# Kernel tuning notes

Hardware: AMD Instinct MI355X
Metric: run time of the kernel (lower is better)

The kernel has to match this reference:

```python
import jax, jax.numpy as jnp
import numpy as np

B, N, D, H = 4, 2048, 1024, 16
DH = D // H

def setup_inputs() -> dict:
    key = jax.random.key(0)
    kx, kqkv, ko = jax.random.split(key, 3)
    x = jax.random.normal(kx, (B, N, D), dtype=jnp.float32)
    # torch Linear weights: [out, in]; scale like default init
    W_qkv = jax.random.normal(kqkv, (3 * D, D), dtype=jnp.float32) * (1.0 / np.sqrt(D))
    W_out = jax.random.normal(ko, (D, D), dtype=jnp.float32) * (1.0 / np.sqrt(D))
    return {"x": x, "W_qkv": W_qkv, "W_out": W_out}

def reference(x, W_qkv, W_out):
    Bk, Nk, C = x.shape
    qkv = jnp.einsum('bnc,oc->bno', x, W_qkv)  # [B,N,3D]
    qkv = qkv.reshape(Bk, Nk, 3, H, DH).transpose(2, 0, 3, 1, 4)  # [3,B,H,N,DH]
    q, k, v = qkv[0], qkv[1], qkv[2]
    att = jnp.einsum('bhnd,bhmd->bhnm', q, k) * (1.0 / np.sqrt(DH))
    mask = jnp.triu(jnp.ones((Nk, Nk), dtype=bool), k=1)  # True above diagonal
    att = jnp.where(mask, -jnp.inf, att)
    att = jax.nn.softmax(att, axis=-1)
    y = jnp.einsum('bhnm,bhmd->bhnd', att, v)  # [B,H,N,DH]
    y = y.transpose(0, 2, 1, 3).reshape(Bk, Nk, C)
    return jnp.einsum('bnc,oc->bno', y, W_out)
```

## Files before the change

kernel.cpp:

```cpp
#include <hip/hip_runtime.h>
#include <hip/hip_bf16.h>
#include <stdint.h>

#define Bb 4
#define Nn 2048
#define Dd 1024
#define Hh 16
#define DHd 64
#define Mm (Bb*Nn)
#define D3 (3*Dd)

typedef unsigned short u16;
typedef unsigned int u32;
typedef __attribute__((ext_vector_type(8))) short bf16x8;
typedef __attribute__((ext_vector_type(4))) float f32x4;
typedef __attribute__((ext_vector_type(2))) unsigned int u32x2;
typedef __attribute__((ext_vector_type(4))) unsigned int u32x4;

__device__ __forceinline__ u16 f2bf(float f) {
    unsigned int u = __float_as_uint(f);
    u = (u + 0x7FFFu + ((u >> 16) & 1u)) >> 16;
    return (u16)u;
}

__device__ __forceinline__ u32 cvtpk_bf16(float lo, float hi) {
    u32 r;
    asm("v_cvt_pk_bf16_f32 %0, %1, %2" : "=v"(r) : "v"(lo), "v"(hi));
    return r;
}

__device__ __forceinline__ float fexp2(float x) {
    float r;
    asm("v_exp_f32 %0, %1" : "=v"(r) : "v"(x));
    return r;
}

#define GLOAD16(g, l)                                                          \
    __builtin_amdgcn_global_load_lds(                                          \
        (const __attribute__((address_space(1))) unsigned int*)(g),            \
        (__attribute__((address_space(3))) unsigned int*)(l), 16, 0, 0)

__global__ void cvt_all(const float* __restrict__ x, const float* __restrict__ wqkv,
                        const float* __restrict__ wout, u16* __restrict__ xb,
                        u16* __restrict__ wqkvb, u16* __restrict__ woutb, float s) {
    const int A4 = Mm * Dd / 4;
    const int B4 = D3 * Dd / 4;
    const int C4 = Dd * Dd / 4;
    const int QCUT = Dd * Dd / 4;
    const int total = A4 + B4 + C4;
    int i = blockIdx.x * blockDim.x + threadIdx.x;
    const int stride = gridDim.x * blockDim.x;
    for (; i < total; i += stride) {
        const float* src; u16* dst; int j; float sc = 1.f;
        if (i < A4) { src = x; dst = xb; j = i; }
        else if (i < A4 + B4) { j = i - A4; src = wqkv; dst = wqkvb; if (j < QCUT) sc = s; }
        else { j = i - A4 - B4; src = wout; dst = woutb; }
        float4 v = ((const float4*)src)[j];
        u16 o0 = f2bf(v.x * sc), o1 = f2bf(v.y * sc), o2 = f2bf(v.z * sc), o3 = f2bf(v.w * sc);
        ((uint2*)dst)[j] = make_uint2((u32)o0 | ((u32)o1 << 16), (u32)o2 | ((u32)o3 << 16));
    }
}

template<int OUT_F32>
__global__ __launch_bounds__(256) void gemm_bt(const u16* __restrict__ A,
                                               const u16* __restrict__ Bm,
                                               void* __restrict__ C,
                                               int M, int Nout, int K) {
    __shared__ u16 As[128 * 64];
    __shared__ u16 Bs[128 * 64];
    const int t = threadIdx.x;
    const int lane = t & 63;
    const int w = t >> 6;
    const int wr = w >> 1, wc = w & 1;
    const int l15 = lane & 15, l4 = lane >> 4;

    const int gx = gridDim.x;
    const int linear = blockIdx.y * gx + blockIdx.x;
    const int cpx = (gx * gridDim.y) >> 3;
    const int tile = (linear & 7) * cpx + (linear >> 3);
    const int m0 = (tile / gx) * 128;
    const int n0 = (tile % gx) * 128;

    f32x4 acc[4][4] = {};

    for (int k0 = 0; k0 < K; k0 += 64) {
        __syncthreads();
#pragma unroll
        for (int i = 0; i < 4; i++) {
            int chunk = i * 256 + t;
            int row = chunk >> 3;
            int csw = ((chunk & 7) ^ (row & 7)) << 3;
            GLOAD16(A + (size_t)(m0 + row) * K + k0 + csw, &As[chunk * 8]);
            GLOAD16(Bm + (size_t)(n0 + row) * K + k0 + csw, &Bs[chunk * 8]);
        }
        __syncthreads();

#pragma unroll
        for (int kh = 0; kh < 2; kh++) {
            bf16x8 a[4], b[4];
#pragma unroll
            for (int mi = 0; mi < 4; mi++) {
                int row = wr * 64 + mi * 16 + l15;
                a[mi] = *(const bf16x8*)&As[row * 64 + (((kh * 4 + l4) ^ (row & 7)) << 3)];
            }
#pragma unroll
            for (int nj = 0; nj < 4; nj++) {
                int row = wc * 64 + nj * 16 + l15;
                b[nj] = *(const bf16x8*)&Bs[row * 64 + (((kh * 4 + l4) ^ (row & 7)) << 3)];
            }
#pragma unroll
            for (int mi = 0; mi < 4; mi++)
#pragma unroll
                for (int nj = 0; nj < 4; nj++)
                    acc[mi][nj] = __builtin_amdgcn_mfma_f32_16x16x32_bf16(a[mi], b[nj], acc[mi][nj], 0, 0, 0);
        }
    }

#pragma unroll
    for (int mi = 0; mi < 4; mi++) {
#pragma unroll
        for (int nj = 0; nj < 4; nj++) {
            int col = n0 + wc * 64 + nj * 16 + l15;
#pragma unroll
            for (int r = 0; r < 4; r++) {
                int row = m0 + wr * 64 + mi * 16 + l4 * 4 + r;
                float v = acc[mi][nj][r];
                if (OUT_F32)
                    ((float*)C)[(size_t)row * Nout + col] = v;
                else
                    ((u16*)C)[(size_t)row * Nout + col] = f2bf(v);
            }
        }
    }
}

__global__ __launch_bounds__(512) void attn(const u16* __restrict__ qkv, u16* __restrict__ y) {
    __shared__ u16 Kt[2][64 * 64];
    __shared__ u16 Vt[2][64 * 64];

    const int t = threadIdx.x;
    const int lane = t & 63;
    const int w = t >> 6;
    const int l15 = lane & 15, l4 = lane >> 4;
    const int bh = blockIdx.x * 8 + (blockIdx.y & 7);
    const int pairidx = blockIdx.y >> 3;
    const int b = bh >> 4, h = bh & 15;

    const u16* qbase = qkv + (size_t)(b * Nn) * D3 + h * DHd;
    const u16* Kg = qbase + Dd;
    const u16* Vg = qbase + 2 * Dd;

    const int krow = t >> 3;
    const int ksw = (((t & 7) ^ (krow & 7)) << 3);
    const int vi = t & 31;
    const int vsd = (t >> 5) * 4;
    const int vchunk = (2 * vi) >> 3;
    const int vcol = (2 * vi) & 7;

    const bool hi2 = (lane >> 5) & 1;
    const bool bit0 = (lane >> 4) & 1;
    const int sgrp = lane & 48;

    bool mgt[4];
#pragma unroll
    for (int r = 0; r < 4; r++) mgt[r] = (l4 * 4 + r) > l15;

    for (int pass = 0; pass < 2; ++pass) {
        const int qt = pass == 0 ? pairidx : (15 - pairidx);
        const int q0 = qt * 128;
        const int ktmax = 2 * qt + 1;
        const int qwmin = q0 + w * 16;

        bf16x8 qf[2];
        {
            const u16* qrow = qbase + (size_t)(qwmin + l15) * D3;
            qf[0] = *(const bf16x8*)(qrow + l4 * 8);
            qf[1] = *(const bf16x8*)(qrow + 32 + l4 * 8);
        }

        f32x4 o[4] = {};
        float m_ = -1e30f;
        float l_ = 0.f;

        u32x2 va, vb_;

        GLOAD16(Kg + (size_t)krow * D3 + ksw, &Kt[0][t * 8]);
        {
            const u16* vr = Vg + (size_t)(2 * vi) * D3 + vsd;
            va = *(const u32x2*)vr;
            vb_ = *(const u32x2*)(vr + D3);
        }
        asm volatile("s_waitcnt vmcnt(0)" ::: "memory");
        {
            u16 av[4], bv[4];
            *(u32x2*)av = va; *(u32x2*)bv = vb_;
#pragma unroll
            for (int j = 0; j < 4; j++) {
                int d = vsd + j;
                u32 word = (u32)av[j] | ((u32)bv[j] << 16);
                *(u32*)&Vt[0][d * 64 + ((vchunk ^ (d & 7)) << 3) + vcol] = word;
            }
        }
        __syncthreads();

        int cur = 0;
        for (int kt = 0; kt <= ktmax; ++kt) {
            const int k0 = kt * 64;
            const int havenext = (kt < ktmax);

            if (havenext) {
                const int nk0 = k0 + 64;
                GLOAD16(Kg + (size_t)(nk0 + krow) * D3 + ksw, &Kt[cur ^ 1][t * 8]);
                const u16* vr = Vg + (size_t)(nk0 + 2 * vi) * D3 + vsd;
                va = *(const u32x2*)vr;
                vb_ = *(const u32x2*)(vr + D3);
            }

            const int dks = (qwmin - k0) >> 4;

            if (dks >= 0) {
                const int kcm = dks < 3 ? dks : 3;
                const int kgm = (dks >> 1) < 1 ? (dks >> 1) : 1;

                f32x4 sv[4];
                float lm = -3.0e38f;
                __builtin_amdgcn_s_setprio(1);
#pragma unroll
                for (int kc = 0; kc < 4; ++kc) {
                    if (kc <= kcm) {
                        f32x4 s = {};
                        int row = kc * 16 + l15;
                        int sw = row & 7;
                        bf16x8 kf0 = *(const bf16x8*)&Kt[cur][row * 64 + ((l4 ^ sw) << 3)];
                        bf16x8 kf1 = *(const bf16x8*)&Kt[cur][row * 64 + (((4 + l4) ^ sw) << 3)];
                        s = __builtin_amdgcn_mfma_f32_16x16x32_bf16(kf0, qf[0], s, 0, 0, 0);
                        s = __builtin_amdgcn_mfma_f32_16x16x32_bf16(kf1, qf[1], s, 0, 0, 0);
                        const bool bmask = (kc == dks);
#pragma unroll
                        for (int r = 0; r < 4; r++) {
                            float x = s[r];
                            if (bmask && mgt[r]) x = -1e30f;
                            sv[kc][r] = x;
                            lm = fmaxf(lm, x);
                        }
                    }
                }
                __builtin_amdgcn_s_setprio(0);

                if (!__all(lm <= m_ + 8.f)) {
                    float vmax = fmaxf(lm, __shfl_xor(lm, 16));
                    vmax = fmaxf(vmax, __shfl_xor(vmax, 32));
                    float newm = fmaxf(m_, vmax);
                    float corr = fexp2(m_ - newm);
                    l_ *= corr;
                    float corr_o[4];
#pragma unroll
                    for (int r = 0; r < 4; ++r)
                        corr_o[r] = __shfl(corr, sgrp | (((lane >> 4) & 3) * 4 + r));
#pragma unroll
                    for (int db = 0; db < 4; db++)
#pragma unroll
                        for (int r = 0; r < 4; r++) o[db][r] *= corr_o[r];
                    m_ = newm;
                }

                u32 up[4][2];
#pragma unroll
                for (int kc = 0; kc < 4; ++kc) {
                    if (kc <= kcm) {
                        float p0 = fexp2(sv[kc][0] - m_);
                        float p1 = fexp2(sv[kc][1] - m_);
                        float p2 = fexp2(sv[kc][2] - m_);
                        float p3 = fexp2(sv[kc][3] - m_);
                        l_ += (p0 + p1) + (p2 + p3);
                        up[kc][0] = cvtpk_bf16(p0, p1);
                        up[kc][1] = cvtpk_bf16(p2, p3);
                    } else {
                        up[kc][0] = 0u;
                        up[kc][1] = 0u;
                    }
                }

                __builtin_amdgcn_s_setprio(1);
#pragma unroll
                for (int kg = 0; kg < 2; kg++) {
                    if (kg <= kgm) {
                        u32 paya0 = hi2 ? up[2 * kg + 1][0] : up[2 * kg][0];
                        u32 paya1 = hi2 ? up[2 * kg + 1][1] : up[2 * kg][1];
                        u32 payb0 = hi2 ? up[2 * kg][0] : up[2 * kg + 1][0];
                        u32 payb1 = hi2 ? up[2 * kg][1] : up[2 * kg + 1][1];
                        u32 a16_0 = (u32)__shfl_xor((int)paya0, 16);
                        u32 a16_1 = (u32)__shfl_xor((int)paya1, 16);
                        u32 a32_0 = (u32)__shfl_xor((int)payb0, 32);
                        u32 a32_1 = (u32)__shfl_xor((int)payb1, 32);
                        u32 a48_0 = (u32)__shfl_xor((int)payb0, 48);
                        u32 a48_1 = (u32)__shfl_xor((int)payb1, 48);
                        u32x4 tt;
                        tt[0] = hi2 ? (bit0 ? a16_0 : a32_0) : (bit0 ? a48_0 : paya0);
                        tt[1] = hi2 ? (bit0 ? a16_1 : a32_1) : (bit0 ? a48_1 : paya1);
                        tt[2] = hi2 ? (bit0 ? paya0 : a48_0) : (bit0 ? a32_0 : a16_0);
                        tt[3] = hi2 ? (bit0 ? paya1 : a48_1) : (bit0 ? a32_1 : a16_1);
                        union { u32x4 u; bf16x8 b; } pa;
                        pa.u = tt;
#pragma unroll
                        for (int db = 0; db < 4; db++) {
                            int d = db * 16 + l15;
                            bf16x8 vb = *(const bf16x8*)&Vt[cur][d * 64 + (((kg * 4 + l4) ^ (d & 7)) << 3)];
                            o[db] = __builtin_amdgcn_mfma_f32_16x16x32_bf16(pa.b, vb, o[db], 0, 0, 0);
                        }
                    }
                }
                __builtin_amdgcn_s_setprio(0);
            }

            if (havenext) {
                asm volatile("s_waitcnt vmcnt(0)" ::: "memory");
                u16 av[4], bv[4];
                *(u32x2*)av = va; *(u32x2*)bv = vb_;
#pragma unroll
                for (int j = 0; j < 4; j++) {
                    int d = vsd + j;
                    u32 word = (u32)av[j] | ((u32)bv[j] << 16);
                    *(u32*)&Vt[cur ^ 1][d * 64 + ((vchunk ^ (d & 7)) << 3) + vcol] = word;
                }
            }
            __syncthreads();
            cur ^= 1;
        }

        l_ += __shfl_xor(l_, 16);
        l_ += __shfl_xor(l_, 32);
        float linv = 1.f / l_;
        float linv_o[4];
#pragma unroll
        for (int r = 0; r < 4; ++r)
            linv_o[r] = __shfl(linv, sgrp | (((lane >> 4) & 3) * 4 + r));
#pragma unroll
        for (int r = 0; r < 4; r++) {
            int qg = qwmin + l4 * 4 + r;
            u16* yrow = y + (size_t)(b * Nn + qg) * Dd + h * DHd;
#pragma unroll
            for (int db = 0; db < 4; db++)
                yrow[db * 16 + l15] = f2bf(o[db][r] * linv_o[r]);
        }
    }
}

extern "C" void kernel_launch(void* const* d_in, const int* in_sizes, int n_in,
                              void* d_out, int out_size, void* d_ws, size_t ws_size,
                              hipStream_t stream) {
    const float* x = (const float*)d_in[0];
    const float* Wqkv = (const float*)d_in[1];
    const float* Wout = (const float*)d_in[2];

    char* ws = (char*)d_ws;
    size_t off = 0;
    u16* xb = (u16*)(ws + off);    off += (size_t)Mm * Dd * 2;
    u16* wqkvb = (u16*)(ws + off); off += (size_t)D3 * Dd * 2;
    u16* woutb = (u16*)(ws + off); off += (size_t)Dd * Dd * 2;
    u16* qkv = (u16*)(ws + off);   off += (size_t)Mm * D3 * 2;
    u16* yb = (u16*)(ws + off);    off += (size_t)Mm * Dd * 2;

    const float SCL = 0.125f * 1.4426950408889634f;

    cvt_all<<<4096, 256, 0, stream>>>(x, Wqkv, Wout, xb, wqkvb, woutb, SCL);

    gemm_bt<0><<<dim3(D3 / 128, Mm / 128), 256, 0, stream>>>(xb, wqkvb, qkv, Mm, D3, Dd);
    attn<<<dim3(8, 64), 512, 0, stream>>>(qkv, yb);
    gemm_bt<1><<<dim3(Dd / 128, Mm / 128), 256, 0, stream>>>(yb, woutb, d_out, Mm, Dd, Dd);
}
```

Before: 172.9 us.

## Switch attention to 32x32x16 MFMA with 4 waves of 32 query rows

Restructures the attention kernel so each of 4 waves (256 threads) handles 32 query rows using 32x32x16 bf16 MFMAs instead of 8 waves of 16 rows with 16x16x32. The P-operand relayout now uses v_permlane32_swap instead of several cross-lane shuffles. The per-row softmax rescale no longer needs broadcast shuffles. Output is staged through LDS so it can be written to global memory as 16-byte stores instead of scattered 2-byte writes. The trade-off is more registers per wave, coarser causal masking granularity (wasted work on diagonal tiles), and an extra LDS round-trip and barrier at the end of each pass.

Measured after the change: 185.3 us. +7.1%, slower.

```diff
diff --git a/kernel.cpp b/kernel.cpp
--- a/kernel.cpp
+++ b/kernel.cpp
@@ -14,7 +14,7 @@
 typedef unsigned int u32;
 typedef __attribute__((ext_vector_type(8))) short bf16x8;
 typedef __attribute__((ext_vector_type(4))) float f32x4;
-typedef __attribute__((ext_vector_type(2))) unsigned int u32x2;
+typedef __attribute__((ext_vector_type(16))) float f32x16;
 typedef __attribute__((ext_vector_type(4))) unsigned int u32x4;
 
 __device__ __forceinline__ u16 f2bf(float f) {
@@ -134,14 +134,15 @@
     }
 }
 
-__global__ __launch_bounds__(512) void attn(const u16* __restrict__ qkv, u16* __restrict__ y) {
+__global__ __launch_bounds__(256, 4) void attn(const u16* __restrict__ qkv, u16* __restrict__ y) {
     __shared__ u16 Kt[2][64 * 64];
     __shared__ u16 Vt[2][64 * 64];
 
     const int t = threadIdx.x;
     const int lane = t & 63;
     const int w = t >> 6;
-    const int l15 = lane & 15, l4 = lane >> 4;
+    const int q31 = lane & 31;
+    const int hi = lane >> 5;
     const int bh = blockIdx.x * 8 + (blockIdx.y & 7);
     const int pairidx = blockIdx.y >> 3;
     const int b = bh >> 4, h = bh & 15;
@@ -150,52 +151,45 @@
     const u16* Kg = qbase + Dd;
     const u16* Vg = qbase + 2 * Dd;
 
-    const int krow = t >> 3;
-    const int ksw = (((t & 7) ^ (krow & 7)) << 3);
+    const int kr0 = t >> 3;
+    const int ks0 = (((t & 7) ^ (kr0 & 7)) << 3);
     const int vi = t & 31;
-    const int vsd = (t >> 5) * 4;
+    const int vsd = (t >> 5) * 8;
     const int vchunk = (2 * vi) >> 3;
     const int vcol = (2 * vi) & 7;
 
-    const bool hi2 = (lane >> 5) & 1;
-    const bool bit0 = (lane >> 4) & 1;
-    const int sgrp = lane & 48;
-
-    bool mgt[4];
-#pragma unroll
-    for (int r = 0; r < 4; r++) mgt[r] = (l4 * 4 + r) > l15;
-
     for (int pass = 0; pass < 2; ++pass) {
-        const int qt = pass == 0 ? pairidx : (15 - pairidx);
+        const int qt = pass ? (15 - pairidx) : pairidx;
         const int q0 = qt * 128;
         const int ktmax = 2 * qt + 1;
-        const int qwmin = q0 + w * 16;
-
-        bf16x8 qf[2];
+        const int qw = q0 + w * 32;
+
+        bf16x8 qf[4];
         {
-            const u16* qrow = qbase + (size_t)(qwmin + l15) * D3;
-            qf[0] = *(const bf16x8*)(qrow + l4 * 8);
-            qf[1] = *(const bf16x8*)(qrow + 32 + l4 * 8);
-        }
-
-        f32x4 o[4] = {};
-        float m_ = -1e30f;
-        float l_ = 0.f;
-
-        u32x2 va, vb_;
-
-        GLOAD16(Kg + (size_t)krow * D3 + ksw, &Kt[0][t * 8]);
+            const u16* qrow = qbase + (size_t)(qw + q31) * D3 + hi * 8;
+            qf[0] = *(const bf16x8*)(qrow);
+            qf[1] = *(const bf16x8*)(qrow + 16);
+            qf[2] = *(const bf16x8*)(qrow + 32);
+            qf[3] = *(const bf16x8*)(qrow + 48);
+        }
+
+        f32x16 o0 = {}, o1 = {};
+        float m_ = -1e30f, l_ = 0.f;
+        u32x4 va, vb_;
+
+        GLOAD16(Kg + (size_t)kr0 * D3 + ks0, &Kt[0][t * 8]);
+        GLOAD16(Kg + (size_t)(kr0 + 32) * D3 + ks0, &Kt[0][(t + 256) * 8]);
         {
             const u16* vr = Vg + (size_t)(2 * vi) * D3 + vsd;
-            va = *(const u32x2*)vr;
-            vb_ = *(const u32x2*)(vr + D3);
+            va = *(const u32x4*)vr;
+            vb_ = *(const u32x4*)(vr + D3);
         }
         asm volatile("s_waitcnt vmcnt(0)" ::: "memory");
         {
-            u16 av[4], bv[4];
-            *(u32x2*)av = va; *(u32x2*)bv = vb_;
-#pragma unroll
-            for (int j = 0; j < 4; j++) {
+            u16 av[8], bv[8];
+            *(u32x4*)av = va; *(u32x4*)bv = vb_;
+#pragma unroll
+            for (int j = 0; j < 8; j++) {
                 int d = vsd + j;
                 u32 word = (u32)av[j] | ((u32)bv[j] << 16);
                 *(u32*)&Vt[0][d * 64 + ((vchunk ^ (d & 7)) << 3) + vcol] = word;
@@ -210,104 +204,120 @@
 
             if (havenext) {
                 const int nk0 = k0 + 64;
-                GLOAD16(Kg + (size_t)(nk0 + krow) * D3 + ksw, &Kt[cur ^ 1][t * 8]);
+                GLOAD16(Kg + (size_t)(nk0 + kr0) * D3 + ks0, &Kt[cur ^ 1][t * 8]);
+                GLOAD16(Kg + (size_t)(nk0 + kr0 + 32) * D3 + ks0, &Kt[cur ^ 1][(t + 256) * 8]);
                 const u16* vr = Vg + (size_t)(nk0 + 2 * vi) * D3 + vsd;
-                va = *(const u32x2*)vr;
-                vb_ = *(const u32x2*)(vr + D3);
-            }
-
-            const int dks = (qwmin - k0) >> 4;
-
-            if (dks >= 0) {
-                const int kcm = dks < 3 ? dks : 3;
-                const int kgm = (dks >> 1) < 1 ? (dks >> 1) : 1;
-
-                f32x4 sv[4];
-                float lm = -3.0e38f;
+                va = *(const u32x4*)vr;
+                vb_ = *(const u32x4*)(vr + D3);
+            }
+
+            const int dq = qw - k0;
+
+            if (dq >= 0) {
+                const int two = (dq >= 32);
+
+                f32x16 s0 = {}, s1 = {};
                 __builtin_amdgcn_s_setprio(1);
 #pragma unroll
-                for (int kc = 0; kc < 4; ++kc) {
-                    if (kc <= kcm) {
-                        f32x4 s = {};
-                        int row = kc * 16 + l15;
-                        int sw = row & 7;
-                        bf16x8 kf0 = *(const bf16x8*)&Kt[cur][row * 64 + ((l4 ^ sw) << 3)];
-                        bf16x8 kf1 = *(const bf16x8*)&Kt[cur][row * 64 + (((4 + l4) ^ sw) << 3)];
-                        s = __builtin_amdgcn_mfma_f32_16x16x32_bf16(kf0, qf[0], s, 0, 0, 0);
-                        s = __builtin_amdgcn_mfma_f32_16x16x32_bf16(kf1, qf[1], s, 0, 0, 0);
-                        const bool bmask = (kc == dks);
-#pragma unroll
-                        for (int r = 0; r < 4; r++) {
-                            float x = s[r];
-                            if (bmask && mgt[r]) x = -1e30f;
-                            sv[kc][r] = x;
-                            lm = fmaxf(lm, x);
-                        }
+                for (int c = 0; c < 4; ++c) {
+                    bf16x8 kf = *(const bf16x8*)&Kt[cur][q31 * 64 + (((2 * c + hi) ^ (q31 & 7)) << 3)];
+                    s0 = __builtin_amdgcn_mfma_f32_32x32x16_bf16(kf, qf[c], s0, 0, 0, 0);
+                }
+                if (two) {
+#pragma unroll
+                    for (int c = 0; c < 4; ++c) {
+                        bf16x8 kf = *(const bf16x8*)&Kt[cur][(32 + q31) * 64 + (((2 * c + hi) ^ (q31 & 7)) << 3)];
+                        s1 = __builtin_amdgcn_mfma_f32_32x32x16_bf16(kf, qf[c], s1, 0, 0, 0);
                     }
                 }
                 __builtin_amdgcn_s_setprio(0);
 
+                if (dq == 0) {
+#pragma unroll
+                    for (int r = 0; r < 16; ++r) {
+                        int krel = (r & 3) + 8 * (r >> 2) + 4 * hi;
+                        if (krel > q31) s0[r] = -1e30f;
+                    }
+                }
+                if (dq == 32) {
+#pragma unroll
+                    for (int r = 0; r < 16; ++r) {
+                        int krel = (r & 3) + 8 * (r >> 2) + 4 * hi;
+                        if (krel > q31) s1[r] = -1e30f;
+                    }
+                }
+
+                float lm = s0[0];
+#pragma unroll
+                for (int r = 1; r < 16; ++r) lm = fmaxf(lm, s0[r]);
+                if (two) {
+#pragma unroll
+                    for (int r = 0; r < 16; ++r) lm = fmaxf(lm, s1[r]);
+                }
+
                 if (!__all(lm <= m_ + 8.f)) {
-                    float vmax = fmaxf(lm, __shfl_xor(lm, 16));
-                    vmax = fmaxf(vmax, __shfl_xor(vmax, 32));
-                    float newm = fmaxf(m_, vmax);
+                    float pm = __shfl_xor(lm, 32);
+                    float vq = fmaxf(lm, pm);
+                    float newm = fmaxf(m_, vq);
                     float corr = fexp2(m_ - newm);
                     l_ *= corr;
-                    float corr_o[4];
-#pragma unroll
-                    for (int r = 0; r < 4; ++r)
-                        corr_o[r] = __shfl(corr, sgrp | (((lane >> 4) & 3) * 4 + r));
-#pragma unroll
-                    for (int db = 0; db < 4; db++)
-#pragma unroll
-                        for (int r = 0; r < 4; r++) o[db][r] *= corr_o[r];
+                    o0 = o0 * corr;
+                    o1 = o1 * corr;
                     m_ = newm;
                 }
 
-                u32 up[4][2];
-#pragma unroll
-                for (int kc = 0; kc < 4; ++kc) {
-                    if (kc <= kcm) {
-                        float p0 = fexp2(sv[kc][0] - m_);
-                        float p1 = fexp2(sv[kc][1] - m_);
-                        float p2 = fexp2(sv[kc][2] - m_);
-                        float p3 = fexp2(sv[kc][3] - m_);
+                u32 wd0[4][2], wd1[4][2];
+#pragma unroll
+                for (int g = 0; g < 4; ++g) {
+                    float p0 = fexp2(s0[4 * g + 0] - m_);
+                    float p1 = fexp2(s0[4 * g + 1] - m_);
+                    float p2 = fexp2(s0[4 * g + 2] - m_);
+                    float p3 = fexp2(s0[4 * g + 3] - m_);
+                    l_ += (p0 + p1) + (p2 + p3);
+                    wd0[g][0] = cvtpk_bf16(p0, p1);
+                    wd0[g][1] = cvtpk_bf16(p2, p3);
+                }
+                if (two) {
+#pragma unroll
+                    for (int g = 0; g < 4; ++g) {
+                        float p0 = fexp2(s1[4 * g + 0] - m_);
+                        float p1 = fexp2(s1[4 * g + 1] - m_);
+                        float p2 = fexp2(s1[4 * g + 2] - m_);
+                        float p3 = fexp2(s1[4 * g + 3] - m_);
                         l_ += (p0 + p1) + (p2 + p3);
-                        up[kc][0] = cvtpk_bf16(p0, p1);
-                        up[kc][1] = cvtpk_bf16(p2, p3);
-                    } else {
-                        up[kc][0] = 0u;
-                        up[kc][1] = 0u;
+                        wd1[g][0] = cvtpk_bf16(p0, p1);
+                        wd1[g][1] = cvtpk_bf16(p2, p3);
                     }
                 }
 
                 __builtin_amdgcn_s_setprio(1);
 #pragma unroll
-                for (int kg = 0; kg < 2; kg++) {
-                    if (kg <= kgm) {
-                        u32 paya0 = hi2 ? up[2 * kg + 1][0] : up[2 * kg][0];
-                        u32 paya1 = hi2 ? up[2 * kg + 1][1] : up[2 * kg][1];
-                        u32 payb0 = hi2 ? up[2 * kg][0] : up[2 * kg + 1][0];
-                        u32 payb1 = hi2 ? up[2 * kg][1] : up[2 * kg + 1][1];
-                        u32 a16_0 = (u32)__shfl_xor((int)paya0, 16);
-                        u32 a16_1 = (u32)__shfl_xor((int)paya1, 16);
-                        u32 a32_0 = (u32)__shfl_xor((int)payb0, 32);
-                        u32 a32_1 = (u32)__shfl_xor((int)payb1, 32);
-                        u32 a48_0 = (u32)__shfl_xor((int)payb0, 48);
-                        u32 a48_1 = (u32)__shfl_xor((int)payb1, 48);
-                        u32x4 tt;
-                        tt[0] = hi2 ? (bit0 ? a16_0 : a32_0) : (bit0 ? a48_0 : paya0);
-                        tt[1] = hi2 ? (bit0 ? a16_1 : a32_1) : (bit0 ? a48_1 : paya1);
-                        tt[2] = hi2 ? (bit0 ? paya0 : a48_0) : (bit0 ? a32_0 : a16_0);
-                        tt[3] = hi2 ? (bit0 ? paya1 : a48_1) : (bit0 ? a32_1 : a16_1);
-                        union { u32x4 u; bf16x8 b; } pa;
-                        pa.u = tt;
-#pragma unroll
-                        for (int db = 0; db < 4; db++) {
-                            int d = db * 16 + l15;
-                            bf16x8 vb = *(const bf16x8*)&Vt[cur][d * 64 + (((kg * 4 + l4) ^ (d & 7)) << 3)];
-                            o[db] = __builtin_amdgcn_mfma_f32_16x16x32_bf16(pa.b, vb, o[db], 0, 0, 0);
-                        }
+                for (int c = 0; c < 2; ++c) {
+                    u32 a0 = wd0[2 * c][0], a1 = wd0[2 * c][1];
+                    u32 b0 = wd0[2 * c + 1][0], b1 = wd0[2 * c + 1][1];
+                    asm("v_permlane32_swap_b32 %0, %1" : "+v"(a0), "+v"(b0));
+                    asm("v_permlane32_swap_b32 %0, %1" : "+v"(a1), "+v"(b1));
+                    union { u32x4 u; bf16x8 f; } pa;
+                    pa.u[0] = a0; pa.u[1] = a1; pa.u[2] = b0; pa.u[3] = b1;
+                    bf16x8 v0 = *(const bf16x8*)&Vt[cur][q31 * 64 + (((2 * c + hi) ^ (q31 & 7)) << 3)];
+                    bf16x8 v1 = *(const bf16x8*)&Vt[cur][(32 + q31) * 64 + (((2 * c + hi) ^ (q31 & 7)) << 3)];
+                    o0 = __builtin_amdgcn_mfma_f32_32x32x16_bf16(v0, pa.f, o0, 0, 0, 0);
+                    o1 = __builtin_amdgcn_mfma_f32_32x32x16_bf16(v1, pa.f, o1, 0, 0, 0);
+                }
+                if (two) {
+#pragma unroll
+                    for (int c = 0; c < 2; ++c) {
+                        u32 a0 = wd1[2 * c][0], a1 = wd1[2 * c][1];
+                        u32 b0 = wd1[2 * c + 1][0], b1 = wd1[2 * c + 1][1];
+                        asm("v_permlane32_swap_b32 %0, %1" : "+v"(a0), "+v"(b0));
+                        asm("v_permlane32_swap_b32 %0, %1" : "+v"(a1), "+v"(b1));
+                        union { u32x4 u; bf16x8 f; } pa;
+                        pa.u[0] = a0; pa.u[1] = a1; pa.u[2] = b0; pa.u[3] = b1;
+                        int ck = 2 * (c + 2) + hi;
+                        bf16x8 v0 = *(const bf16x8*)&Vt[cur][q31 * 64 + ((ck ^ (q31 & 7)) << 3)];
+                        bf16x8 v1 = *(const bf16x8*)&Vt[cur][(32 + q31) * 64 + ((ck ^ (q31 & 7)) << 3)];
+                        o0 = __builtin_amdgcn_mfma_f32_32x32x16_bf16(v0, pa.f, o0, 0, 0, 0);
+                        o1 = __builtin_amdgcn_mfma_f32_32x32x16_bf16(v1, pa.f, o1, 0, 0, 0);
                     }
                 }
                 __builtin_amdgcn_s_setprio(0);
@@ -315,10 +325,10 @@
 
             if (havenext) {
                 asm volatile("s_waitcnt vmcnt(0)" ::: "memory");
-                u16 av[4], bv[4];
-                *(u32x2*)av = va; *(u32x2*)bv = vb_;
-#pragma unroll
-                for (int j = 0; j < 4; j++) {
+                u16 av[8], bv[8];
+                *(u32x4*)av = va; *(u32x4*)bv = vb_;
+#pragma unroll
+                for (int j = 0; j < 8; j++) {
                     int d = vsd + j;
                     u32 word = (u32)av[j] | ((u32)bv[j] << 16);
                     *(u32*)&Vt[cur ^ 1][d * 64 + ((vchunk ^ (d & 7)) << 3) + vcol] = word;
@@ -328,21 +338,37 @@
             cur ^= 1;
         }
 
-        l_ += __shfl_xor(l_, 16);
-        l_ += __shfl_xor(l_, 32);
-        float linv = 1.f / l_;
-        float linv_o[4];
-#pragma unroll
-        for (int r = 0; r < 4; ++r)
-            linv_o[r] = __shfl(linv, sgrp | (((lane >> 4) & 3) * 4 + r));
-#pragma unroll
-        for (int r = 0; r < 4; r++) {
-            int qg = qwmin + l4 * 4 + r;
-            u16* yrow = y + (size_t)(b * Nn + qg) * Dd + h * DHd;
-#pragma unroll
-            for (int db = 0; db < 4; db++)
-                yrow[db * 16 + l15] = f2bf(o[db][r] * linv_o[r]);
-        }
+        float lq = l_ + __shfl_xor(l_, 32);
+        float linv = 1.f / lq;
+        u16* Ep = ((u16*)&Kt[0][0]) + w * 2048;
+#pragma unroll
+        for (int dt = 0; dt < 2; ++dt) {
+#pragma unroll
+            for (int g = 0; g < 4; ++g) {
+#pragma unroll
+                for (int s2 = 0; s2 < 2; ++s2) {
+                    float e0 = (dt ? o1[4 * g + 2 * s2] : o0[4 * g + 2 * s2]) * linv;
+                    float e1 = (dt ? o1[4 * g + 2 * s2 + 1] : o0[4 * g + 2 * s2 + 1]) * linv;
+                    u32 word = cvtpk_bf16(e0, e1);
+                    int chnk = 4 * dt + g;
+                    int off = q31 * 64 + ((chnk ^ (q31 & 7)) << 3) + 4 * hi + 2 * s2;
+                    *(u32*)&Ep[off] = word;
+                }
+            }
+        }
+        asm volatile("s_waitcnt lgkmcnt(0)" ::: "memory");
+        {
+            int qp = lane >> 1;
+            int dh = lane & 1;
+            u16* yrow = y + (size_t)(b * Nn + qw + qp) * Dd + h * DHd + dh * 32;
+#pragma unroll
+            for (int cc = 0; cc < 4; ++cc) {
+                int chnk = dh * 4 + cc;
+                u32x4 vv = *(const u32x4*)&Ep[(qp - q31) * 0 + qp * 64 + ((chnk ^ (qp & 7)) << 3)];
+                *(u32x4*)(yrow + cc * 8) = vv;
+            }
+        }
+        __syncthreads();
     }
 }
 
@@ -366,6 +392,6 @@
     cvt_all<<<4096, 256, 0, stream>>>(x, Wqkv, Wout, xb, wqkvb, woutb, SCL);
 
     gemm_bt<0><<<dim3(D3 / 128, Mm / 128), 256, 0, stream>>>(xb, wqkvb, qkv, Mm, D3, Dd);
-    attn<<<dim3(8, 64), 512, 0, stream>>>(qkv, yb);
+    attn<<<dim3(8, 64), 256, 0, stream>>>(qkv, yb);
     gemm_bt<1><<<dim3(Dd / 128, Mm / 128), 256, 0, stream>>>(yb, woutb, d_out, Mm, Dd, Dd);
 }
```
